# Optimization experiments

Hardware: AMD Instinct MI355X
Metric: run time of the kernel (lower is better)

Reference implementation:

```python
import jax, jax.numpy as jnp
import numpy as np

B, H, T, DH = 4, 8, 4096, 128
BUCKETS = 32


def setup_inputs() -> dict:
    key = jax.random.key(0)
    k1, k2, k3, k4 = jax.random.split(key, 4)
    q = jax.random.normal(k1, (B, H, T, DH), jnp.float32)
    k = jax.random.normal(k2, (B, H, T, DH), jnp.float32)
    v = jax.random.normal(k3, (B, H, T, DH), jnp.float32)
    W_sort = jax.random.normal(k4, (1, H, 2 * DH, BUCKETS), jnp.float32)
    return {"q": q, "k": k, "v": v, "W_sort": W_sort}


def _build_mask(h, buckets, bsz):
    hh = h // 2
    i = jnp.arange(bsz)[:, None]
    j = jnp.arange(2 * bsz)[None, :]
    # reordered-bucket half (j < bsz) fully visible; current bucket causal
    causal = (j < bsz) | (i >= (j - bsz))  # [bsz, 2*bsz]
    # rotated heads, last bucket: rows > 0 cannot see first bsz+1 cols; row 0 can
    special = (j <= bsz) & (i > 0)
    last_rot = causal & ~special
    mask = jnp.broadcast_to(causal, (h, buckets, bsz, 2 * bsz))
    mask = mask.at[hh:, -1].set(last_rot)
    return mask  # [h, buckets, bsz, 2*bsz] bool


def reference(q, k, v, W_sort):
    b, h, t, d_h = q.shape
    buckets = W_sort.shape[-1]
    d = h * d_h  # full model dim, used for the attention scale
    bsz = t // buckets
    hh = h // 2

    def rot(x, n):
        # rotate only the second half of heads along time
        return jnp.concatenate([x[:, :hh], jnp.roll(x[:, hh:], n, axis=2)], axis=1)

    q = rot(q, -(bsz - 1))
    k = rot(k, -(bsz - 1))
    v = rot(v, -(bsz - 1))

    bq = q.reshape(b, h, buckets, bsz, d_h)
    bk = k.reshape(b, h, buckets, bsz, d_h)
    bv = v.reshape(b, h, buckets, bsz, d_h)

    # --- sort net: cumulative-average key features of first token per bucket ---
    r = jnp.arange(1, t + 1, dtype=k.dtype)
    kc = jnp.cumsum(k, axis=2) / r[None, None, :, None]
    kr = jnp.concatenate([kc, k], axis=-1).reshape(b, h, buckets, bsz, 2 * d_h)
    x = kr[:, :, :, 0]  # [b, h, buckets, 2*d_h]
    R = jax.nn.leaky_relu(jnp.einsum('bhue,hev->bhuv', x, W_sort[0]))
    R = jax.nn.softmax(R, axis=-1)
    R = jnp.tril(R, -1)
    # keep only the top-1 entry per row (first argmax, like torch.topk k=1)
    idx = jnp.argmax(R, axis=-1)
    R = jnp.max(R, axis=-1, keepdims=True) * jax.nn.one_hot(idx, buckets, dtype=R.dtype)

    # --- permutation gather of one past bucket of k/v per query bucket ---
    k_re = jnp.einsum('bhuv,bhvtd->bhutd', R, bk)
    v_re = jnp.einsum('bhuv,bhvtd->bhutd', R, bv)
    bk2 = jnp.concatenate([k_re, bk], axis=3)  # [b,h,buckets,2*bsz,d_h]
    bv2 = jnp.concatenate([v_re, bv], axis=3)

    dots = jnp.einsum('bhuie,bhuje->bhuij', bq, bk2) * (float(d) ** -0.5)
    mask = _build_mask(h, buckets, bsz)
    neg = -jnp.finfo(dots.dtype).max
    dots = jnp.where(mask[None], dots, neg)
    attn = jax.nn.softmax(dots, axis=-1)
    out = jnp.einsum('bhuij,bhuje->bhuie', attn, bv2)
    out = out.reshape(b, h, t, d_h)
    out = rot(out, bsz - 1)
    return out
```

## Files before the change

### kernel.cpp

```cpp
#include <hip/hip_runtime.h>

constexpr int T_    = 4096;
constexpr int DH_   = 128;
constexpr int NB_   = 32;
constexpr int BSZ_  = 128;
constexpr int HH_   = 4;
constexpr int H_    = 8;
constexpr int BH_   = 32;

typedef __attribute__((ext_vector_type(8))) short short8;
typedef __attribute__((ext_vector_type(4))) float f32x4;

__device__ __forceinline__ unsigned int cvt_pk_bf16(float lo, float hi) {
  unsigned int r;
  asm("v_cvt_pk_bf16_f32 %0, %1, %2" : "=v"(r) : "v"(lo), "v"(hi));
  return r;
}

__global__ __launch_bounds__(256)
void k_bucket_sums(const float* __restrict__ k,
                   float* __restrict__ bucketsum,
                   float* __restrict__ firstrow) {
  __shared__ float4 red[8][32];
  int blk = blockIdx.x;
  int u = blk & (NB_ - 1);
  int bh = blk >> 5;
  int h = bh & (H_ - 1);
  bool rot = (h >= HH_);
  int tid = threadIdx.x;
  int rq = tid >> 5;
  int l  = tid & 31;
  int d0 = l * 4;
  const float* kb = k + (size_t)bh * T_ * DH_;

  float4 s = {0.f, 0.f, 0.f, 0.f};
  float4 first = {0.f, 0.f, 0.f, 0.f};
  #pragma unroll
  for (int it = 0; it < 16; ++it) {
    int i = it * 8 + rq;
    int t = u * BSZ_ + i;
    if (rot) t = (t + (BSZ_ - 1)) & (T_ - 1);
    float4 a = *(const float4*)(kb + (size_t)t * DH_ + d0);
    s.x += a.x; s.y += a.y; s.z += a.z; s.w += a.w;
    if (it == 0 && rq == 0) first = a;
  }
  red[rq][l] = s;
  __syncthreads();
  if (rq == 0) {
    float4 acc = {0.f, 0.f, 0.f, 0.f};
    #pragma unroll
    for (int j = 0; j < 8; ++j) {
      float4 a = red[j][l];
      acc.x += a.x; acc.y += a.y; acc.z += a.z; acc.w += a.w;
    }
    *(float4*)(bucketsum + (size_t)blk * DH_ + d0) = acc;
    *(float4*)(firstrow  + (size_t)blk * DH_ + d0) = first;
  }
}

__global__ __launch_bounds__(256)
void k_routing(const float* __restrict__ W,
               const float* __restrict__ bucketsum,
               const float* __restrict__ firstrow,
               float2* __restrict__ scIdx) {
  __shared__ float Wl[2 * DH_ * NB_];
  __shared__ float Xl[NB_][2 * DH_ + 1];
  __shared__ float Rl[NB_][36];
  int bh = blockIdx.x;
  int h = bh & (H_ - 1);
  int tid = threadIdx.x;

  const float4* Wg = (const float4*)(W + (size_t)h * 2 * DH_ * NB_);
  #pragma unroll
  for (int rep = 0; rep < 8; ++rep)
    ((float4*)Wl)[tid + rep * 256] = Wg[tid + rep * 256];

  if (tid < DH_) {
    int d = tid;
    float S = 0.f;
    for (int u = 0; u < NB_; ++u) {
      float fr = firstrow [((size_t)bh * NB_ + u) * DH_ + d];
      float bs = bucketsum[((size_t)bh * NB_ + u) * DH_ + d];
      Xl[u][d]        = (S + fr) / (float)(u * BSZ_ + 1);
      Xl[u][DH_ + d]  = fr;
      S += bs;
    }
  }
  __syncthreads();

  {
    int u = tid >> 3;
    int vg = tid & 7;
    float4 racc = {0.f, 0.f, 0.f, 0.f};
    for (int e = 0; e < 2 * DH_; ++e) {
      float xv = Xl[u][e];
      float4 wv = *(const float4*)(Wl + e * NB_ + vg * 4);
      racc.x += xv * wv.x; racc.y += xv * wv.y;
      racc.z += xv * wv.z; racc.w += xv * wv.w;
    }
    racc.x = (racc.x > 0.f) ? racc.x : 0.01f * racc.x;
    racc.y = (racc.y > 0.f) ? racc.y : 0.01f * racc.y;
    racc.z = (racc.z > 0.f) ? racc.z : 0.01f * racc.z;
    racc.w = (racc.w > 0.f) ? racc.w : 0.01f * racc.w;
    *(float4*)(&Rl[u][vg * 4]) = racc;
  }
  __syncthreads();

  if (tid < NB_) {
    int u = tid;
    float m = -3.4e38f;
    float r[NB_];
    #pragma unroll
    for (int v = 0; v < NB_; ++v) { r[v] = Rl[u][v]; m = fmaxf(m, r[v]); }
    float Z = 0.f;
    #pragma unroll
    for (int v = 0; v < NB_; ++v) Z += expf(r[v] - m);
    float best = -3.4e38f; int bi = 0;
    for (int v = 0; v < u; ++v) {
      if (r[v] > best) { best = r[v]; bi = v; }
    }
    float sc = (u == 0) ? 0.f : expf(best - m) / Z;
    int  idx = (u == 0) ? 0 : bi;
    scIdx[bh * NB_ + u] = make_float2(sc, __int_as_float(idx));
  }
}

__global__ __launch_bounds__(512, 4)
void k_attn(const float* __restrict__ q, const float* __restrict__ k,
            const float* __restrict__ v, const float2* __restrict__ scIdx,
            float* __restrict__ out) {
  __shared__ __align__(16) unsigned short RA[128 * 128];
  __shared__ __align__(16) unsigned short RB[128 * 128];

  int blk0 = blockIdx.x;
  int blk  = ((blk0 & 7) << 7) | (blk0 >> 3);
  int u  = blk & (NB_ - 1);
  int bh = blk >> 5;
  int h  = bh & (H_ - 1);
  bool rot = (h >= HH_);
  float2 si = scIdx[bh * NB_ + u];
  float sc = si.x;
  int  src = __float_as_int(si.y);
  const size_t base = (size_t)bh * T_ * DH_;

  int tid  = threadIdx.x;
  int lane = tid & 63;
  int w    = tid >> 6;
  int g    = lane >> 4;
  int c    = lane & 15;

  short8 qf[4];
  {
    int t = u * BSZ_ + 16 * w + c;
    if (rot) t = (t + (BSZ_ - 1)) & (T_ - 1);
    const float* qrow = q + base + (size_t)t * DH_;
    #pragma unroll
    for (int kt = 0; kt < 4; ++kt) {
      f32x4 a = *(const f32x4*)(qrow + kt * 32 + g * 8);
      f32x4 b = *(const f32x4*)(qrow + kt * 32 + g * 8 + 4);
      union { unsigned int u32[4]; short8 s; } U;
      U.u32[0] = cvt_pk_bf16(a[0], a[1]);
      U.u32[1] = cvt_pk_bf16(a[2], a[3]);
      U.u32[2] = cvt_pk_bf16(b[0], b[1]);
      U.u32[3] = cvt_pk_bf16(b[2], b[3]);
      qf[kt] = U.s;
    }
  }

  #pragma unroll
  for (int rep = 0; rep < 16; ++rep) {
    int chunk = tid + rep * 512;
    int jr = chunk >> 5;
    int c0 = (chunk & 31) * 4;
    int t = (jr < BSZ_) ? (src * BSZ_ + jr) : (u * BSZ_ + (jr - BSZ_));
    if (rot) t = (t + (BSZ_ - 1)) & (T_ - 1);
    f32x4 a = *(const f32x4*)(k + base + (size_t)t * DH_ + c0);
    uint2 wv;
    wv.x = cvt_pk_bf16(a[0], a[1]);
    wv.y = cvt_pk_bf16(a[2], a[3]);
    unsigned short* Rg = (jr < BSZ_) ? RA : RB;
    int row = jr & 127;
    *(uint2*)((char*)Rg + row * 256 + ((c0 * 2) ^ ((row & 15) << 4))) = wv;
  }
  __syncthreads();

  f32x4 acc[16];
  #pragma unroll
  for (int jt = 0; jt < 16; ++jt) acc[jt] = f32x4{0.f, 0.f, 0.f, 0.f};

  __builtin_amdgcn_s_setprio(1);
  #pragma unroll
  for (int kt = 0; kt < 4; ++kt) {
    #pragma unroll
    for (int jt = 0; jt < 16; ++jt) {
      const unsigned short* Rg = (jt < 8) ? RA : RB;
      int row = (jt & 7) * 16 + c;
      short8 bfr = *(const short8*)((const char*)Rg + row * 256 + ((kt * 64 + g * 16) ^ ((row & 15) << 4)));
      acc[jt] = __builtin_amdgcn_mfma_f32_16x16x32_bf16(bfr, qf[kt], acc[jt], 0, 0, 0);
    }
  }
  __builtin_amdgcn_s_setprio(0);

  __syncthreads();

  auto vt_stage = [&](int sb, unsigned short* Rg) {
    #pragma unroll
    for (int rep = 0; rep < 2; ++rep) {
      int j0 = ((tid >> 5) + rep * 16) * 4;
      int jc0 = (j0 & ~31) | (((j0 >> 2) & 3) << 3) | (((j0 >> 4) & 1) << 2);
      int d0 = (tid & 31) * 4;
      f32x4 rr[4];
      #pragma unroll
      for (int jj = 0; jj < 4; ++jj) {
        int t = sb * BSZ_ + j0 + jj;
        if (rot) t = (t + (BSZ_ - 1)) & (T_ - 1);
        rr[jj] = *(const f32x4*)(v + base + (size_t)t * DH_ + d0);
      }
      #pragma unroll
      for (int m = 0; m < 4; ++m) {
        uint2 wv;
        wv.x = cvt_pk_bf16(rr[0][m], rr[1][m]);
        wv.y = cvt_pk_bf16(rr[2][m], rr[3][m]);
        int row = d0 + m;
        *(uint2*)((char*)Rg + row * 256 + ((jc0 * 2) ^ ((row & 15) << 4))) = wv;
      }
    }
  };

  vt_stage(src, RA);

  const bool lastrot = rot && (u == NB_ - 1);
  const float LOG2E = 1.44269504f;
  float scale1 = 0.03125f * LOG2E * sc;
  float scale2 = 0.03125f * LOG2E;
  const int i = 16 * w + c;
  const bool killLow = lastrot && (i > 0);

  float mx = -3.4e38f;
  #pragma unroll
  for (int jt = 0; jt < 16; ++jt) {
    #pragma unroll
    for (int r = 0; r < 4; ++r) {
      float s = acc[jt][r] * ((jt < 8) ? scale1 : scale2);
      bool vis;
      if (jt < 8) {
        vis = !killLow;
      } else {
        int jb = 16 * (jt - 8) + 4 * g + r;
        vis = (i >= jb);
        if (jt == 8) vis = vis && !(killLow && (g == 0) && (r == 0));
      }
      s = vis ? s : -3.4e38f;
      acc[jt][r] = s;
      mx = fmaxf(mx, s);
    }
  }
  mx = fmaxf(mx, __shfl_xor(mx, 16));
  mx = fmaxf(mx, __shfl_xor(mx, 32));
  float zs = 0.f;
  #pragma unroll
  for (int jt = 0; jt < 16; ++jt) {
    #pragma unroll
    for (int r = 0; r < 4; ++r) {
      float p = exp2f(acc[jt][r] - mx);
      acc[jt][r] = p;
      zs += p;
    }
  }
  zs += __shfl_xor(zs, 16);
  zs += __shfl_xor(zs, 32);
  float rz = 1.f / zs;
  float rzs = rz * sc;

  vt_stage(u, RB);

  union { short8 s8[8]; unsigned int u32[32]; } PA;
  #pragma unroll
  for (int m = 0; m < 8; ++m) {
    #pragma unroll
    for (int qq = 0; qq < 4; ++qq) {
      int jt = 2 * m + (qq >> 1);
      int wsel = qq & 1;
      float f = (jt < 8) ? rzs : rz;
      PA.u32[4 * m + qq] = cvt_pk_bf16(acc[jt][2 * wsel] * f, acc[jt][2 * wsel + 1] * f);
    }
  }
  __syncthreads();

  f32x4 o[8];
  #pragma unroll
  for (int nt = 0; nt < 8; ++nt) o[nt] = f32x4{0.f, 0.f, 0.f, 0.f};

  __builtin_amdgcn_s_setprio(1);
  #pragma unroll
  for (int m = 0; m < 8; ++m) {
    const unsigned short* Rg = (m < 4) ? RA : RB;
    int mloc = m & 3;
    #pragma unroll
    for (int nt = 0; nt < 8; ++nt) {
      int vrow = nt * 16 + c;
      short8 vb = *(const short8*)((const char*)Rg + vrow * 256 + ((mloc * 64 + g * 16) ^ ((vrow & 15) << 4)));
      o[nt] = __builtin_amdgcn_mfma_f32_16x16x32_bf16(PA.s8[m], vb, o[nt], 0, 0, 0);
    }
  }
  __builtin_amdgcn_s_setprio(0);

  #pragma unroll
  for (int r = 0; r < 4; ++r) {
    int il = 4 * g + r;
    int t = u * BSZ_ + 16 * w + il;
    if (rot) t = (t + (BSZ_ - 1)) & (T_ - 1);
    float* orow = out + base + (size_t)t * DH_;
    #pragma unroll
    for (int nt = 0; nt < 8; ++nt) {
      orow[nt * 16 + c] = o[nt][r];
    }
  }
}

extern "C" void kernel_launch(void* const* d_in, const int* in_sizes, int n_in,
                              void* d_out, int out_size, void* d_ws, size_t ws_size,
                              hipStream_t stream) {
  const float* q = (const float*)d_in[0];
  const float* k = (const float*)d_in[1];
  const float* v = (const float*)d_in[2];
  const float* W = (const float*)d_in[3];
  float* out = (float*)d_out;

  float*  bucketsum = (float*)d_ws;
  float*  firstrow  = bucketsum + 131072;
  float2* scIdx     = (float2*)(firstrow + 131072);

  k_bucket_sums<<<BH_ * NB_, 256, 0, stream>>>(k, bucketsum, firstrow);
  k_routing<<<BH_, 256, 0, stream>>>(W, bucketsum, firstrow, scIdx);
  k_attn<<<BH_ * NB_, 512, 0, stream>>>(q, k, v, scIdx, out);
}
```

Measured before the change: 89.07 us.

## Split attention into two halves with online softmax merge to cut registers

```diff
diff --git a/kernel.cpp b/kernel.cpp
--- a/kernel.cpp
+++ b/kernel.cpp
@@ -182,25 +182,6 @@
     int row = jr & 127;
     *(uint2*)((char*)Rg + row * 256 + ((c0 * 2) ^ ((row & 15) << 4))) = wv;
   }
-  __syncthreads();
-
-  f32x4 acc[16];
-  #pragma unroll
-  for (int jt = 0; jt < 16; ++jt) acc[jt] = f32x4{0.f, 0.f, 0.f, 0.f};
-
-  __builtin_amdgcn_s_setprio(1);
-  #pragma unroll
-  for (int kt = 0; kt < 4; ++kt) {
-    #pragma unroll
-    for (int jt = 0; jt < 16; ++jt) {
-      const unsigned short* Rg = (jt < 8) ? RA : RB;
-      int row = (jt & 7) * 16 + c;
-      short8 bfr = *(const short8*)((const char*)Rg + row * 256 + ((kt * 64 + g * 16) ^ ((row & 15) << 4)));
-      acc[jt] = __builtin_amdgcn_mfma_f32_16x16x32_bf16(bfr, qf[kt], acc[jt], 0, 0, 0);
-    }
-  }
-  __builtin_amdgcn_s_setprio(0);
-
   __syncthreads();
 
   auto vt_stage = [&](int sb, unsigned short* Rg) {
@@ -227,64 +208,132 @@
     }
   };
 
-  vt_stage(src, RA);
-
   const bool lastrot = rot && (u == NB_ - 1);
   const float LOG2E = 1.44269504f;
-  float scale1 = 0.03125f * LOG2E * sc;
-  float scale2 = 0.03125f * LOG2E;
+  const float scale1 = 0.03125f * LOG2E * sc;
+  const float scale2 = 0.03125f * LOG2E;
   const int i = 16 * w + c;
   const bool killLow = lastrot && (i > 0);
 
-  float mx = -3.4e38f;
-  #pragma unroll
-  for (int jt = 0; jt < 16; ++jt) {
+  f32x4 acc[8];
+  #pragma unroll
+  for (int jt = 0; jt < 8; ++jt) acc[jt] = f32x4{0.f, 0.f, 0.f, 0.f};
+  __builtin_amdgcn_s_setprio(1);
+  #pragma unroll
+  for (int kt = 0; kt < 4; ++kt) {
+    #pragma unroll
+    for (int jt = 0; jt < 8; ++jt) {
+      int row = jt * 16 + c;
+      short8 bfr = *(const short8*)((const char*)RA + row * 256 + ((kt * 64 + g * 16) ^ ((row & 15) << 4)));
+      acc[jt] = __builtin_amdgcn_mfma_f32_16x16x32_bf16(bfr, qf[kt], acc[jt], 0, 0, 0);
+    }
+  }
+  __builtin_amdgcn_s_setprio(0);
+  __syncthreads();
+
+  vt_stage(src, RA);
+
+  float m1 = -3.4e38f;
+  #pragma unroll
+  for (int jt = 0; jt < 8; ++jt) {
     #pragma unroll
     for (int r = 0; r < 4; ++r) {
-      float s = acc[jt][r] * ((jt < 8) ? scale1 : scale2);
-      bool vis;
-      if (jt < 8) {
-        vis = !killLow;
-      } else {
-        int jb = 16 * (jt - 8) + 4 * g + r;
-        vis = (i >= jb);
-        if (jt == 8) vis = vis && !(killLow && (g == 0) && (r == 0));
-      }
-      s = vis ? s : -3.4e38f;
+      float s = acc[jt][r] * scale1;
+      s = killLow ? -3.4e38f : s;
       acc[jt][r] = s;
-      mx = fmaxf(mx, s);
-    }
-  }
-  mx = fmaxf(mx, __shfl_xor(mx, 16));
-  mx = fmaxf(mx, __shfl_xor(mx, 32));
-  float zs = 0.f;
-  #pragma unroll
-  for (int jt = 0; jt < 16; ++jt) {
+      m1 = fmaxf(m1, s);
+    }
+  }
+  m1 = fmaxf(m1, __shfl_xor(m1, 16));
+  m1 = fmaxf(m1, __shfl_xor(m1, 32));
+  float z1 = 0.f;
+  #pragma unroll
+  for (int jt = 0; jt < 8; ++jt) {
     #pragma unroll
     for (int r = 0; r < 4; ++r) {
-      float p = exp2f(acc[jt][r] - mx);
+      float p = exp2f(acc[jt][r] - m1);
       acc[jt][r] = p;
-      zs += p;
-    }
-  }
-  zs += __shfl_xor(zs, 16);
-  zs += __shfl_xor(zs, 32);
-  float rz = 1.f / zs;
-  float rzs = rz * sc;
-
-  vt_stage(u, RB);
-
-  union { short8 s8[8]; unsigned int u32[32]; } PA;
-  #pragma unroll
-  for (int m = 0; m < 8; ++m) {
+      z1 += p;
+    }
+  }
+  z1 += __shfl_xor(z1, 16);
+  z1 += __shfl_xor(z1, 32);
+
+  union { short8 s8[4]; unsigned int u32[16]; } PA1;
+  #pragma unroll
+  for (int m = 0; m < 4; ++m) {
     #pragma unroll
     for (int qq = 0; qq < 4; ++qq) {
       int jt = 2 * m + (qq >> 1);
       int wsel = qq & 1;
-      float f = (jt < 8) ? rzs : rz;
-      PA.u32[4 * m + qq] = cvt_pk_bf16(acc[jt][2 * wsel] * f, acc[jt][2 * wsel + 1] * f);
-    }
-  }
+      PA1.u32[4 * m + qq] = cvt_pk_bf16(acc[jt][2 * wsel], acc[jt][2 * wsel + 1]);
+    }
+  }
+
+  #pragma unroll
+  for (int jt = 0; jt < 8; ++jt) acc[jt] = f32x4{0.f, 0.f, 0.f, 0.f};
+  __builtin_amdgcn_s_setprio(1);
+  #pragma unroll
+  for (int kt = 0; kt < 4; ++kt) {
+    #pragma unroll
+    for (int jt = 0; jt < 8; ++jt) {
+      int row = jt * 16 + c;
+      short8 bfr = *(const short8*)((const char*)RB + row * 256 + ((kt * 64 + g * 16) ^ ((row & 15) << 4)));
+      acc[jt] = __builtin_amdgcn_mfma_f32_16x16x32_bf16(bfr, qf[kt], acc[jt], 0, 0, 0);
+    }
+  }
+  __builtin_amdgcn_s_setprio(0);
+
+  float m2 = -3.4e38f;
+  #pragma unroll
+  for (int jt = 0; jt < 8; ++jt) {
+    #pragma unroll
+    for (int r = 0; r < 4; ++r) {
+      int jb = 16 * jt + 4 * g + r;
+      float s = acc[jt][r] * scale2;
+      bool vis = (i >= jb);
+      if (jt == 0) vis = vis && !(killLow && (g == 0) && (r == 0));
+      s = vis ? s : -3.4e38f;
+      acc[jt][r] = s;
+      m2 = fmaxf(m2, s);
+    }
+  }
+  m2 = fmaxf(m2, __shfl_xor(m2, 16));
+  m2 = fmaxf(m2, __shfl_xor(m2, 32));
+  float z2 = 0.f;
+  #pragma unroll
+  for (int jt = 0; jt < 8; ++jt) {
+    #pragma unroll
+    for (int r = 0; r < 4; ++r) {
+      float p = exp2f(acc[jt][r] - m2);
+      acc[jt][r] = p;
+      z2 += p;
+    }
+  }
+  z2 += __shfl_xor(z2, 16);
+  z2 += __shfl_xor(z2, 32);
+
+  float mfull = fmaxf(m1, m2);
+  float e1 = exp2f(m1 - mfull);
+  float e2 = exp2f(m2 - mfull);
+  float z  = z1 * e1 + z2 * e2;
+  float rz = 1.f / z;
+  float f1 = sc * e1 * rz;
+  float f2 = e2 * rz;
+
+  union { short8 s8[4]; unsigned int u32[16]; } PA2;
+  #pragma unroll
+  for (int m = 0; m < 4; ++m) {
+    #pragma unroll
+    for (int qq = 0; qq < 4; ++qq) {
+      int jt = 2 * m + (qq >> 1);
+      int wsel = qq & 1;
+      PA2.u32[4 * m + qq] = cvt_pk_bf16(acc[jt][2 * wsel] * f2, acc[jt][2 * wsel + 1] * f2);
+    }
+  }
+  __syncthreads();
+
+  vt_stage(u, RB);
   __syncthreads();
 
   f32x4 o[8];
@@ -293,14 +342,31 @@
 
   __builtin_amdgcn_s_setprio(1);
   #pragma unroll
-  for (int m = 0; m < 8; ++m) {
-    const unsigned short* Rg = (m < 4) ? RA : RB;
-    int mloc = m & 3;
+  for (int m = 0; m < 4; ++m) {
     #pragma unroll
     for (int nt = 0; nt < 8; ++nt) {
       int vrow = nt * 16 + c;
-      short8 vb = *(const short8*)((const char*)Rg + vrow * 256 + ((mloc * 64 + g * 16) ^ ((vrow & 15) << 4)));
-      o[nt] = __builtin_amdgcn_mfma_f32_16x16x32_bf16(PA.s8[m], vb, o[nt], 0, 0, 0);
+      short8 vb = *(const short8*)((const char*)RA + vrow * 256 + ((m * 64 + g * 16) ^ ((vrow & 15) << 4)));
+      o[nt] = __builtin_amdgcn_mfma_f32_16x16x32_bf16(PA1.s8[m], vb, o[nt], 0, 0, 0);
+    }
+  }
+  __builtin_amdgcn_s_setprio(0);
+
+  #pragma unroll
+  for (int r = 0; r < 4; ++r) {
+    float fr = __shfl(f1, 4 * g + r);
+    #pragma unroll
+    for (int nt = 0; nt < 8; ++nt) o[nt][r] *= fr;
+  }
+
+  __builtin_amdgcn_s_setprio(1);
+  #pragma unroll
+  for (int m = 0; m < 4; ++m) {
+    #pragma unroll
+    for (int nt = 0; nt < 8; ++nt) {
+      int vrow = nt * 16 + c;
+      short8 vb = *(const short8*)((const char*)RB + vrow * 256 + ((m * 64 + g * 16) ^ ((vrow & 15) << 4)));
+      o[nt] = __builtin_amdgcn_mfma_f32_16x16x32_bf16(PA2.s8[m], vb, o[nt], 0, 0, 0);
     }
   }
   __builtin_amdgcn_s_setprio(0);
```

Measured after the change: 109.7 us. +23.1%, slower.
